# Performance work log

Hardware: AMD Instinct MI355X
Metric: run time of the kernel (lower is better)

The kernel has to match this reference:

```python
import jax, jax.numpy as jnp
import numpy as np
from jax import lax
import math

N_QUBITS = 10
N_LAYERS = 4
PI = jnp.float32(math.pi)


def _c(x):
    return x.astype(jnp.complex64)


def rx_mat(t):
    c = _c(jnp.cos(0.5 * t)); s = _c(jnp.sin(0.5 * t))
    return jnp.stack([jnp.stack([c, -1j * s]), jnp.stack([-1j * s, c])])


def ry_mat(t):
    c = _c(jnp.cos(0.5 * t)); s = _c(jnp.sin(0.5 * t))
    return jnp.stack([jnp.stack([c, -s]), jnp.stack([s, c])])


def rz_mat(t):
    e0 = jnp.exp(_c(jnp.zeros_like(t)) - 0.5j * _c(t))
    e1 = jnp.exp(0.5j * _c(t))
    z = jnp.zeros_like(e0)
    return jnp.stack([jnp.stack([e0, z]), jnp.stack([z, e1])])


def apply_1q(psi, U, q):
    # psi: (2,)*n complex, apply 2x2 U on axis q
    psi = jnp.moveaxis(psi, q, 0)
    psi = jnp.tensordot(U, psi, axes=(1, 0))
    return jnp.moveaxis(psi, 0, q)


def apply_cnot(psi, ctrl, tgt):
    psi = jnp.moveaxis(psi, (ctrl, tgt), (0, 1))
    a00, a01, a10, a11 = psi[0, 0], psi[0, 1], psi[1, 0], psi[1, 1]
    psi = jnp.stack([jnp.stack([a00, a01]), jnp.stack([a11, a10])])
    return jnp.moveaxis(psi, (0, 1), (ctrl, tgt))


def vqc(state, weights):
    # state: (D,) float32 angles; weights: (layers, n, 3)
    n, L = N_QUBITS, N_LAYERS
    D = state.shape[0]
    psi = jnp.full((2,) * n, 2.0 ** (-n / 2.0), dtype=jnp.complex64)  # H^n |0>
    for layer in range(L):
        for q in range(n):
            ang = state[(layer * n + q) % D]
            psi = apply_1q(psi, rx_mat(ang), q)
            psi = apply_1q(psi, ry_mat(ang), q)
            psi = apply_1q(psi, rz_mat(weights[layer, q, 0]), q)
            psi = apply_1q(psi, ry_mat(weights[layer, q, 1]), q)
            psi = apply_1q(psi, rz_mat(weights[layer, q, 2]), q)
        for q in range(n - 1):
            psi = apply_cnot(psi, q, q + 1)
        psi = apply_cnot(psi, n - 1, 0)
    probs = jnp.real(psi * jnp.conj(psi))  # (2,)*n
    zdiag = jnp.array([1.0, -1.0], dtype=jnp.float32)
    exps = [jnp.sum(probs * zdiag.reshape((1,) * q + (2,) + (1,) * (n - q - 1)))
            for q in range(n)]
    return jnp.stack(exps)  # (n,)


def lstm_forward(x, W_ih, W_hh, b_ih, b_hh):
    # x: [B,T,Din]; PyTorch gate order: i, f, g, o
    B, T, _ = x.shape
    H = W_hh.shape[1]
    b = b_ih + b_hh

    def step(carry, xt):
        h, c = carry
        gates = xt @ W_ih.T + h @ W_hh.T + b
        i, f, g, o = jnp.split(gates, 4, axis=-1)
        i = jax.nn.sigmoid(i); f = jax.nn.sigmoid(f)
        g = jnp.tanh(g); o = jax.nn.sigmoid(o)
        c = f * c + i * g
        h = o * jnp.tanh(c)
        return (h, c), h

    h0 = jnp.zeros((B, H), x.dtype)
    c0 = jnp.zeros((B, H), x.dtype)
    _, hs = lax.scan(step, (h0, c0), jnp.swapaxes(x, 0, 1))
    return jnp.swapaxes(hs, 0, 1)  # [B,T,H]


def _forward(s, lstm_s, W_ih, W_hh, b_ih, b_hh, proj_W, proj_b,
             in_proj_W, in_proj_b, out_proj_W, out_proj_b,
             qweights, W1, b1, W2, b2):
    hs = lstm_forward(lstm_s, W_ih, W_hh, b_ih, b_hh)      # [B,T,H]
    lstm_last = hs[:, -1, :]                               # [B,H]
    state_full = jnp.concatenate([lstm_last, s], axis=1)   # [B,E]
    lstm_proj = hs @ proj_W.T + proj_b                     # [B,T,E]
    E = proj_W.shape[0]
    Wq, Wk, Wv = in_proj_W[:E], in_proj_W[E:2 * E], in_proj_W[2 * E:]
    bq, bk, bv = in_proj_b[:E], in_proj_b[E:2 * E], in_proj_b[2 * E:]
    q = state_full @ Wq.T + bq                             # [B,E] (1 query token)
    k = lstm_proj @ Wk.T + bk                              # [B,T,E]
    v = lstm_proj @ Wv.T + bv
    scale = 1.0 / jnp.sqrt(jnp.float32(E))                 # num_heads=1 -> head_dim=E
    attn = jax.nn.softmax(jnp.einsum('be,bte->bt', q, k) * scale, axis=-1)
    ctx = jnp.einsum('bt,bte->be', attn, v)
    attn_out = ctx @ out_proj_W.T + out_proj_b             # [B,E]
    merged_state = jnp.concatenate([attn_out, s], axis=1)  # [B,E+F]
    state_norm = jnp.tanh(merged_state) * PI
    qfeat = jax.vmap(lambda st: vqc(st, qweights))(state_norm)  # [B,n]
    merged = jnp.concatenate([merged_state, qfeat], axis=1)
    x = jax.nn.relu(merged @ W1.T + b1)
    return x @ W2.T + b2


def setup_inputs() -> dict:
    key = jax.random.key(0)
    ks = jax.random.split(key, 16)
    B, T = 512, 256
    Din, H, F = 128, 256, 64
    E = H + F          # 320 = state_dim
    Dm = E + F         # 384 = merged_state dim
    n_l1, n_act = 512, 8

    def g(k, shape, std):
        return (std * jax.random.normal(k, shape)).astype(jnp.float32)

    return {
        's': jax.random.normal(ks[0], (B, F), jnp.float32),
        'lstm_s': jax.random.normal(ks[1], (B, T, Din), jnp.float32),
        'W_ih': g(ks[2], (4 * H, Din), 0.05),
        'W_hh': g(ks[3], (4 * H, H), 0.05),
        'b_ih': jnp.zeros((4 * H,), jnp.float32),
        'b_hh': jnp.zeros((4 * H,), jnp.float32),
        'proj_W': g(ks[4], (E, H), 0.05),
        'proj_b': 0.1 * jnp.ones((E,), jnp.float32),
        'in_proj_W': g(ks[5], (3 * E, E), 0.05),
        'in_proj_b': jnp.zeros((3 * E,), jnp.float32),
        'out_proj_W': g(ks[6], (E, E), 0.05),
        'out_proj_b': jnp.zeros((E,), jnp.float32),
        'qweights': jax.random.uniform(ks[7], (N_LAYERS, N_QUBITS, 3), jnp.float32, 0.0, 2.0 * math.pi),
        'W1': g(ks[8], (n_l1, Dm + N_QUBITS), 0.05),
        'b1': 0.1 * jnp.ones((n_l1,), jnp.float32),
        'W2': g(ks[9], (n_act, n_l1), 0.05),
        'b2': 0.1 * jnp.ones((n_act,), jnp.float32),
    }


def reference(s, lstm_s, W_ih, W_hh, b_ih, b_hh, proj_W, proj_b,
              in_proj_W, in_proj_b, out_proj_W, out_proj_b,
              qweights, W1, b1, W2, b2):
    return _forward(s, lstm_s, W_ih, W_hh, b_ih, b_hh, proj_W, proj_b,
                    in_proj_W, in_proj_b, out_proj_W, out_proj_b,
                    qweights, W1, b1, W2, b2)
```

## Files before the change

kernel.cpp:

```cpp
#include <hip/hip_runtime.h>
#include <hip/hip_bf16.h>
#include <math.h>

typedef unsigned int u32;
typedef unsigned long long u64;
typedef unsigned short u16;
typedef __attribute__((ext_vector_type(8))) short short8;
typedef __attribute__((ext_vector_type(4))) float f32x4;
typedef __attribute__((ext_vector_type(4))) int v4i;

#define PI_F 3.14159265358979f
#define B_   512
#define T_   256
#define DIN  128
#define H_   256
#define G4   1024
#define F_   64
#define E_   320
#define DM   384
#define NL1  512
#define NACT 8
#define KMLP 394

__device__ v4i llvm_amdgcn_raw_buffer_load_v4i32(v4i rsrc, int voffset,
                                                 int soffset, int aux)
    __asm("llvm.amdgcn.raw.buffer.load.v4i32");
__device__ void llvm_amdgcn_raw_buffer_store_i32(int vdata, v4i rsrc,
                                                 int voffset, int soffset,
                                                 int aux)
    __asm("llvm.amdgcn.raw.buffer.store.i32");

__device__ __forceinline__ v4i make_srd(const void* p) {
  v4i r;
  r.x = (int)(u32)(u64)p;
  r.y = (int)(u32)((u64)p >> 32);
  r.z = (int)0xFFFFFFFFu;
  r.w = 0x00020000;
  return r;
}

__device__ __forceinline__ float b2f(u16 h) {
  union { u32 u; float f; } v; v.u = ((u32)h) << 16; return v.f;
}
__device__ __forceinline__ u16 f2b(float f) {
  union { float f; u32 u; } v; v.f = f;
  u32 r = (v.u + 0x7FFFu + ((v.u >> 16) & 1u)) >> 16;
  return (u16)r;
}
__device__ __forceinline__ float sigf(float x) { return 1.0f / (1.0f + __expf(-x)); }
__device__ __forceinline__ float tanhfast(float x) { return 2.0f / (1.0f + __expf(-2.0f * x)) - 1.0f; }
__device__ __forceinline__ float2 cmul(float2 a, float2 b) {
  return make_float2(a.x * b.x - a.y * b.y, a.x * b.y + a.y * b.x);
}
__device__ __forceinline__ float2 cadd(float2 a, float2 b) {
  return make_float2(a.x + b.x, a.y + b.y);
}

__global__ void k_prep1(const float* __restrict__ lstm_s,
                        const float* __restrict__ W_ih,
                        const float* __restrict__ W_hh,
                        const float* __restrict__ b_ih,
                        const float* __restrict__ b_hh,
                        const float* __restrict__ ipw,
                        const float* __restrict__ ipb,
                        const float* __restrict__ projb,
                        const float* __restrict__ qw,
                        const float* __restrict__ W1,
                        u16* __restrict__ xbf,
                        u16* __restrict__ hs,
                        u16* __restrict__ Wg,
                        float* __restrict__ bb,
                        float* __restrict__ W1t,
                        float* __restrict__ uw,
                        float* __restrict__ bkp,
                        float* __restrict__ bvp,
                        u32* __restrict__ cnt) {
  const int bid = blockIdx.x;
  const int tid = threadIdx.x;
  if (bid < 8192) {
    u32 u = (u32)bid * 256u + tid;
    u32 c8 = u & 15u, b = (u >> 4) & 511u, t = u >> 13;
    const float* src = lstm_s + ((size_t)b * T_ + t) * DIN + c8 * 8;
    union { u16 h[8]; uint4 v; } tmp;
#pragma unroll
    for (int i = 0; i < 8; ++i) tmp.h[i] = f2b(src[i]);
    *(uint4*)(xbf + ((size_t)t * B_ + b) * DIN + c8 * 8) = tmp.v;
  } else if (bid < 8384) {
    u32 u = (u32)(bid - 8192) * 256u + tid;
    u32 c8 = u % 48u, r = u / 48u;
    const float* src = (c8 < 16) ? (W_ih + (size_t)r * DIN + c8 * 8)
                                 : (W_hh + (size_t)r * H_ + (c8 - 16) * 8);
    union { u16 h[8]; uint4 v; } tmp;
#pragma unroll
    for (int i = 0; i < 8; ++i) tmp.h[i] = f2b(src[i]);
    *(uint4*)(Wg + (size_t)r * 384 + c8 * 8) = tmp.v;
  } else if (bid < 8448) {
    u32 u = (u32)(bid - 8384) * 256u + tid;
    ((uint4*)hs)[u] = make_uint4(0, 0, 0, 0);
  } else if (bid < 9236) {
    u32 u = (u32)(bid - 8448) * 256u + tid;
    u32 k = u / 512u, nn = u % 512u;
    W1t[u] = W1[(size_t)nn * KMLP + k];
  } else if (bid == 9236) {
    for (int i = tid; i < 1024; i += 256) bb[i] = b_ih[i] + b_hh[i];
    for (int i = tid; i < 1024; i += 256) cnt[i] = 0u;
    if (tid < 40) {
      float w0 = qw[tid * 3 + 0], w1 = qw[tid * 3 + 1], w2 = qw[tid * 3 + 2];
      float c0 = cosf(0.5f * w0), s0 = sinf(0.5f * w0);
      float c1 = cosf(0.5f * w1), s1 = sinf(0.5f * w1);
      float c2 = cosf(0.5f * w2), s2 = sinf(0.5f * w2);
      float2 e0m = make_float2(c0, -s0), e0p = make_float2(c0, s0);
      float2 e2m = make_float2(c2, -s2), e2p = make_float2(c2, s2);
      float2 t00 = make_float2(c1 * e0m.x, c1 * e0m.y);
      float2 t01 = make_float2(-s1 * e0p.x, -s1 * e0p.y);
      float2 t10 = make_float2(s1 * e0m.x, s1 * e0m.y);
      float2 t11 = make_float2(c1 * e0p.x, c1 * e0p.y);
      float2 u00 = cmul(e2m, t00), u01 = cmul(e2m, t01);
      float2 u10 = cmul(e2p, t10), u11 = cmul(e2p, t11);
      float* o = uw + tid * 8;
      o[0] = u00.x; o[1] = u00.y; o[2] = u01.x; o[3] = u01.y;
      o[4] = u10.x; o[5] = u10.y; o[6] = u11.x; o[7] = u11.y;
    }
  } else if (bid <= 9238) {
    int o = (bid - 9237) * 256 + tid;
    if (o < E_) {
      float acc = ipb[E_ + o];
      for (int e = 0; e < E_; ++e) acc += ipw[(size_t)(E_ + o) * E_ + e] * projb[e];
      bkp[o] = acc;
    }
  } else {
    int o = (bid - 9239) * 256 + tid;
    if (o < E_) {
      float acc = ipb[2 * E_ + o];
      for (int e = 0; e < E_; ++e) acc += ipw[(size_t)(2 * E_ + o) * E_ + e] * projb[e];
      bvp[o] = acc;
    }
  }
}

__global__ void k_prep2(const float* __restrict__ ipw, const float* __restrict__ projW,
                        float* __restrict__ Wkp, float* __restrict__ Wvp) {
  int bid = blockIdx.x, tid = threadIdx.x;
  int o = (bid < 320) ? bid : (bid - 320);
  const float* wrow = ipw + (size_t)((bid < 320 ? E_ : 2 * E_) + o) * E_;
  float acc = 0.f;
  for (int e = 0; e < E_; ++e) acc += wrow[e] * projW[(size_t)e * H_ + tid];
  (bid < 320 ? Wkp : Wvp)[(size_t)o * H_ + tid] = acc;
}

__global__ void k_prep3(const float* __restrict__ ipw, const float* __restrict__ ipb,
                        const float* __restrict__ opw, const float* __restrict__ opb,
                        const float* __restrict__ Wkp, const float* __restrict__ Wvp,
                        const float* __restrict__ bkp, const float* __restrict__ bvp,
                        float* __restrict__ WuT, float* __restrict__ bu,
                        float* __restrict__ wd, float* __restrict__ ddp,
                        float* __restrict__ Wovt, float* __restrict__ bov) {
  int bid = blockIdx.x, tid = threadIdx.x;
  if (bid < 320) {
    int e = bid;
    float acc = 0.f;
    for (int o = 0; o < E_; ++o) acc += Wkp[(size_t)o * H_ + tid] * ipw[(size_t)o * E_ + e];
    WuT[(size_t)e * H_ + tid] = acc;
  } else if (bid < 576) {
    int jj = bid - 320;
    for (int i = tid; i < E_; i += 256) {
      float acc = 0.f;
      for (int o = 0; o < E_; ++o) acc += opw[(size_t)i * E_ + o] * Wvp[(size_t)o * H_ + jj];
      Wovt[(size_t)jj * E_ + i] = acc;
    }
  } else {
    {
      float acc = 0.f;
      for (int o = 0; o < E_; ++o) acc += Wkp[(size_t)o * H_ + tid] * ipb[o];
      bu[tid] = acc;
    }
    for (int idx = tid; idx < E_; idx += 256) {
      float a1 = 0.f, a2 = opb[idx];
      for (int o = 0; o < E_; ++o) {
        a1 += ipw[(size_t)o * E_ + idx] * bkp[o];
        a2 += opw[(size_t)idx * E_ + o] * bvp[o];
      }
      wd[idx] = a1; bov[idx] = a2;
    }
    if (tid == 0) {
      float acc = 0.f;
      for (int o = 0; o < E_; ++o) acc += ipb[o] * bkp[o];
      ddp[0] = acc;
    }
  }
}

struct LstmArgs {
  const u16* xbf; u16* hs; const u16* Wg; const float* bb; u32* cnt;
};

__launch_bounds__(256, 1)
__global__ void k_lstm(LstmArgs A) {
  const int g   = blockIdx.x & 7;
  const int n   = blockIdx.x >> 3;
  const int tid = threadIdx.x;
  const int wid = tid >> 6, lane = tid & 63;
  __shared__ __align__(16) u16 Wl[32 * 392];

  for (int idx = tid; idx < 32 * 48; idx += 256) {
    int ln = idx / 48, c8 = idx % 48;
    int gr = (ln >> 3) * 256 + n * 8 + (ln & 7);
    *(uint4*)&Wl[ln * 392 + c8 * 8] = *(const uint4*)&A.Wg[(size_t)gr * 384 + c8 * 8];
  }
  const int j  = lane & 7;
  const int gc = n * 8 + j;
  const float bbi = A.bb[gc], bbf2 = A.bb[256 + gc];
  const float bbg = A.bb[512 + gc], bbo = A.bb[768 + gc];

  const int quad = lane >> 4;
  const int mrow = lane & 15;
  const int brow = g * 64 + wid * 16 + mrow;
  const int erow0 = g * 64 + wid * 16 + quad * 4;
  const bool hi = (lane & 8) != 0;
  float crs[4] = {0.f, 0.f, 0.f, 0.f};
  u32* mycnt = A.cnt + g * 64;
  u32 target = 0;

  const v4i hs_srd = make_srd(A.hs);
  const int hvoff = (brow * H_ + quad * 8) * 2;

  uint4 xc0, xc1, xc2, xc3, xn0, xn1, xn2, xn3;
  {
    const u16* xb = A.xbf + ((size_t)0 * B_ + brow) * DIN + quad * 8;
    xc0 = *(const uint4*)(xb + 0);
    xc1 = *(const uint4*)(xb + 32);
    xc2 = *(const uint4*)(xb + 64);
    xc3 = *(const uint4*)(xb + 96);
  }
  __syncthreads();

  for (int t = 0; t < T_; ++t) {
    const int hsoff = t * (B_ * H_ * 2);
    uint4 h0 = __builtin_bit_cast(uint4, llvm_amdgcn_raw_buffer_load_v4i32(hs_srd, hvoff +   0, hsoff, 17));
    uint4 h1 = __builtin_bit_cast(uint4, llvm_amdgcn_raw_buffer_load_v4i32(hs_srd, hvoff +  64, hsoff, 17));
    uint4 h2 = __builtin_bit_cast(uint4, llvm_amdgcn_raw_buffer_load_v4i32(hs_srd, hvoff + 128, hsoff, 17));
    uint4 h3 = __builtin_bit_cast(uint4, llvm_amdgcn_raw_buffer_load_v4i32(hs_srd, hvoff + 192, hsoff, 17));
    uint4 h4 = __builtin_bit_cast(uint4, llvm_amdgcn_raw_buffer_load_v4i32(hs_srd, hvoff + 256, hsoff, 17));
    uint4 h5 = __builtin_bit_cast(uint4, llvm_amdgcn_raw_buffer_load_v4i32(hs_srd, hvoff + 320, hsoff, 17));
    uint4 h6 = __builtin_bit_cast(uint4, llvm_amdgcn_raw_buffer_load_v4i32(hs_srd, hvoff + 384, hsoff, 17));
    uint4 h7 = __builtin_bit_cast(uint4, llvm_amdgcn_raw_buffer_load_v4i32(hs_srd, hvoff + 448, hsoff, 17));
    {
      const int tn = (t + 1 < T_) ? (t + 1) : t;
      const u16* xb = A.xbf + ((size_t)tn * B_ + brow) * DIN + quad * 8;
      xn0 = *(const uint4*)(xb + 0);
      xn1 = *(const uint4*)(xb + 32);
      xn2 = *(const uint4*)(xb + 64);
      xn3 = *(const uint4*)(xb + 96);
    }

    f32x4 acc0 = {0.f, 0.f, 0.f, 0.f}, acc1 = {0.f, 0.f, 0.f, 0.f};
#define MMSTEP(AV, KOFF)                                                          \
    {                                                                             \
      short8 av  = __builtin_bit_cast(short8, AV);                                \
      short8 bv0 = __builtin_bit_cast(short8,                                     \
          *(const uint4*)&Wl[mrow * 392 + (KOFF) + quad * 8]);                    \
      short8 bv1 = __builtin_bit_cast(short8,                                     \
          *(const uint4*)&Wl[(16 + mrow) * 392 + (KOFF) + quad * 8]);             \
      acc0 = __builtin_amdgcn_mfma_f32_16x16x32_bf16(av, bv0, acc0, 0, 0, 0);     \
      acc1 = __builtin_amdgcn_mfma_f32_16x16x32_bf16(av, bv1, acc1, 0, 0, 0);     \
    }
    MMSTEP(xc0, 0)   MMSTEP(xc1, 32)  MMSTEP(xc2, 64)  MMSTEP(xc3, 96)
    MMSTEP(h0, 128)  MMSTEP(h1, 160)  MMSTEP(h2, 192)  MMSTEP(h3, 224)
    MMSTEP(h4, 256)  MMSTEP(h5, 288)  MMSTEP(h6, 320)  MMSTEP(h7, 352)
#undef MMSTEP

    const int hsoff_o = (t + 1) * (B_ * H_ * 2);
#pragma unroll
    for (int r = 0; r < 4; ++r) {
      float x0 = acc0[r], x1v = acc1[r];
      float y0 = __shfl_xor(x0, 8, 64);
      float y1 = __shfl_xor(x1v, 8, 64);
      float iv = (hi ? y0 : x0) + bbi;
      float fv = (hi ? x0 : y0) + bbf2;
      float gv = (hi ? y1 : x1v) + bbg;
      float ov = (hi ? x1v : y1) + bbo;
      float cc = sigf(fv) * crs[r] + sigf(iv) * tanhfast(gv);
      crs[r] = cc;
      float hh = sigf(ov) * tanhfast(cc);
      float hh2 = __shfl_xor(hh, 1, 64);
      if (!hi && ((j & 1) == 0)) {
        u32 pk = (u32)f2b(hh) | ((u32)f2b(hh2) << 16);
        llvm_amdgcn_raw_buffer_store_i32((int)pk, hs_srd,
                                         ((erow0 + r) * H_ + gc) * 2, hsoff_o, 17);
      }
    }
    target += 32;
    if (t != T_ - 1) {
      __syncthreads();
      if (tid == 0) {
        __hip_atomic_fetch_add(mycnt, 1u, __ATOMIC_RELAXED, __HIP_MEMORY_SCOPE_AGENT);
        int guard = 0;
        while (__hip_atomic_load(mycnt, __ATOMIC_RELAXED, __HIP_MEMORY_SCOPE_AGENT) < target) {
          __builtin_amdgcn_s_sleep(1);
          if (++guard > (1 << 24)) break;
        }
      }
      __syncthreads();
      xc0 = xn0; xc1 = xn1; xc2 = xn2; xc3 = xn3;
    }
  }
}

__global__ void k_u(const u16* __restrict__ hs, const float* __restrict__ s,
                    const float* __restrict__ WuT, const float* __restrict__ bu,
                    const float* __restrict__ wd, const float* __restrict__ ddp,
                    float* __restrict__ u, float* __restrict__ dvec) {
  int b = blockIdx.x, tid = threadIdx.x;
  __shared__ float z[E_];
  __shared__ float red[256];
  z[tid] = b2f(hs[((size_t)T_ * B_ + b) * H_ + tid]);
  if (tid < F_) z[H_ + tid] = s[(size_t)b * F_ + tid];
  __syncthreads();
  float acc = bu[tid];
  for (int e = 0; e < E_; ++e) acc += WuT[(size_t)e * H_ + tid] * z[e];
  u[(size_t)b * H_ + tid] = acc;
  float p = 0.f;
  for (int e = tid; e < E_; e += 256) p += wd[e] * z[e];
  red[tid] = p;
  __syncthreads();
  for (int s2 = 128; s2 > 0; s2 >>= 1) {
    if (tid < s2) red[tid] += red[tid + s2];
    __syncthreads();
  }
  if (tid == 0) dvec[b] = red[0] + ddp[0];
}

__global__ void k_aw(const u16* __restrict__ hs, const float* __restrict__ u,
                     const float* __restrict__ dvec, float* __restrict__ wv) {
  int b = blockIdx.x, tid = threadIdx.x;
  int wid = tid >> 6, lane = tid & 63;
  __shared__ float sc[T_];
  __shared__ float red[256];
  const float db = dvec[b];
  const float scale = 0.055901699437494745f;
  float4 ul = *(const float4*)&u[(size_t)b * H_ + lane * 4];
  for (int tt = 0; tt < 64; ++tt) {
    int t = wid * 64 + tt;
    u32 rw0 = ((const u32*)(hs + ((size_t)(t + 1) * B_ + b) * H_))[lane * 2];
    u32 rw1 = ((const u32*)(hs + ((size_t)(t + 1) * B_ + b) * H_))[lane * 2 + 1];
    union { u32 uu; float f; } f0, f1, f2, f3;
    f0.uu = rw0 << 16; f1.uu = rw0 & 0xFFFF0000u;
    f2.uu = rw1 << 16; f3.uu = rw1 & 0xFFFF0000u;
    float p = f0.f * ul.x + f1.f * ul.y + f2.f * ul.z + f3.f * ul.w;
#pragma unroll
    for (int off = 32; off > 0; off >>= 1) p += __shfl_xor(p, off, 64);
    if (lane == 0) sc[t] = (p + db) * scale;
  }
  __syncthreads();
  float v = sc[tid];
  red[tid] = v;
  __syncthreads();
  for (int s2 = 128; s2 > 0; s2 >>= 1) {
    if (tid < s2) red[tid] = fmaxf(red[tid], red[tid + s2]);
    __syncthreads();
  }
  float m = red[0];
  __syncthreads();
  float e = __expf(v - m);
  red[tid] = e;
  __syncthreads();
  for (int s2 = 128; s2 > 0; s2 >>= 1) {
    if (tid < s2) red[tid] += red[tid + s2];
    __syncthreads();
  }
  float inv = 1.f / red[0];
  __syncthreads();
  sc[tid] = e * inv;
  __syncthreads();
  float acc = 0.f;
#pragma unroll 8
  for (int t = 0; t < T_; ++t) {
    acc += sc[t] * b2f(hs[((size_t)(t + 1) * B_ + b) * H_ + tid]);
  }
  wv[(size_t)b * H_ + tid] = acc;
}

__global__ void k_ao(const float* __restrict__ wv, const float* __restrict__ Wovt,
                     const float* __restrict__ bov, const float* __restrict__ s,
                     float* __restrict__ mst) {
  int b = blockIdx.x, tid = threadIdx.x;
  __shared__ float wl[H_];
  if (tid < H_) wl[tid] = wv[(size_t)b * H_ + tid];
  __syncthreads();
  if (tid < E_) {
    float acc = bov[tid];
    for (int jj = 0; jj < H_; ++jj) acc += Wovt[(size_t)jj * E_ + tid] * wl[jj];
    mst[(size_t)b * DM + tid] = acc;
  } else if (tid < DM) {
    mst[(size_t)b * DM + tid] = s[(size_t)b * F_ + (tid - E_)];
  }
}

__global__ void k_vqc(const float* __restrict__ mst, const float* __restrict__ uwg,
                      float* __restrict__ qf) {
  int b = blockIdx.x, tid = threadIdx.x;
  __shared__ float2 psi[1024];
  __shared__ float ang[40];
  __shared__ float uwl[320];
  __shared__ float part[4][10];
  if (tid < 40) ang[tid] = tanhf(mst[(size_t)b * DM + tid]) * PI_F;
  uwl[tid] = uwg[tid];
  if (tid < 64) uwl[256 + tid] = uwg[256 + tid];
#pragma unroll
  for (int k = 0; k < 4; ++k) psi[tid + k * 256] = make_float2(0.03125f, 0.f);
  __syncthreads();
  for (int l = 0; l < 4; ++l) {
    for (int q = 0; q < 10; ++q) {
      int lq = l * 10 + q;
      float a = ang[lq];
      float ca = __cosf(0.5f * a), sa = __sinf(0.5f * a);
      float cs = ca * sa;
      float2 m00 = make_float2(ca * ca, sa * sa);
      float2 m01 = make_float2(-cs, -cs);
      float2 m10 = make_float2(cs, -cs);
      float2 m11 = make_float2(ca * ca, -sa * sa);
      const float* uwp = &uwl[lq * 8];
      float2 a00 = make_float2(uwp[0], uwp[1]), a01 = make_float2(uwp[2], uwp[3]);
      float2 a10 = make_float2(uwp[4], uwp[5]), a11 = make_float2(uwp[6], uwp[7]);
      float2 u00 = cadd(cmul(a00, m00), cmul(a01, m10));
      float2 u01 = cadd(cmul(a00, m01), cmul(a01, m11));
      float2 u10 = cadd(cmul(a10, m00), cmul(a11, m10));
      float2 u11 = cadd(cmul(a10, m01), cmul(a11, m11));
      int bp = 9 - q;
      __syncthreads();
#pragma unroll
      for (int k = 0; k < 2; ++k) {
        int p = tid + k * 256;
        int i0 = ((p >> bp) << (bp + 1)) | (p & ((1 << bp) - 1));
        int i1 = i0 | (1 << bp);
        float2 A0 = psi[i0], A1 = psi[i1];
        psi[i0] = cadd(cmul(u00, A0), cmul(u01, A1));
        psi[i1] = cadd(cmul(u10, A0), cmul(u11, A1));
      }
    }
    for (int q = 0; q < 9; ++q) {
      int lo = 8 - q;
      __syncthreads();
      int p = tid;
      int i0 = ((p >> lo) << (lo + 2)) | (2 << lo) | (p & ((1 << lo) - 1));
      int i1 = i0 | (1 << lo);
      float2 tmp = psi[i0]; psi[i0] = psi[i1]; psi[i1] = tmp;
    }
    __syncthreads();
    {
      int i0 = (tid << 1) | 1;
      int i1 = i0 | 512;
      float2 tmp = psi[i0]; psi[i0] = psi[i1]; psi[i1] = tmp;
    }
  }
  __syncthreads();
  float acc[10];
#pragma unroll
  for (int q = 0; q < 10; ++q) acc[q] = 0.f;
#pragma unroll
  for (int k = 0; k < 4; ++k) {
    int idx = tid + k * 256;
    float2 A = psi[idx];
    float pr = A.x * A.x + A.y * A.y;
#pragma unroll
    for (int q = 0; q < 10; ++q) acc[q] += ((idx >> (9 - q)) & 1) ? -pr : pr;
  }
  int lane = tid & 63, wid = tid >> 6;
#pragma unroll
  for (int q = 0; q < 10; ++q) {
    float vq = acc[q];
#pragma unroll
    for (int off = 32; off > 0; off >>= 1) vq += __shfl_xor(vq, off, 64);
    if (lane == 0) part[wid][q] = vq;
  }
  __syncthreads();
  if (tid < 10) qf[(size_t)b * 10 + tid] = part[0][tid] + part[1][tid] + part[2][tid] + part[3][tid];
}

__global__ void k_mlp(const float* __restrict__ mst, const float* __restrict__ qf,
                      const float* __restrict__ W1t, const float* __restrict__ b1,
                      const float* __restrict__ W2, const float* __restrict__ b2,
                      float* __restrict__ out) {
  int b = blockIdx.x, tid = threadIdx.x;
  __shared__ float mg[KMLP];
  __shared__ float x1[NL1];
  __shared__ float red[256];
  for (int i = tid; i < DM; i += 256) mg[i] = mst[(size_t)b * DM + i];
  if (tid < 10) mg[DM + tid] = qf[(size_t)b * 10 + tid];
  __syncthreads();
#pragma unroll
  for (int hh = 0; hh < 2; ++hh) {
    int nn = tid + hh * 256;
    float acc = b1[nn];
#pragma unroll 4
    for (int k = 0; k < KMLP; ++k) acc += W1t[(size_t)k * NL1 + nn] * mg[k];
    x1[nn] = fmaxf(acc, 0.f);
  }
  __syncthreads();
  int a = tid >> 5, l32 = tid & 31;
  float p = 0.f;
  for (int k = l32; k < NL1; k += 32) p += x1[k] * W2[(size_t)a * NL1 + k];
  red[tid] = p;
  __syncthreads();
  if (tid < 8) {
    float acc = b2[tid];
#pragma unroll
    for (int i = 0; i < 32; ++i) acc += red[tid * 32 + i];
    out[(size_t)b * NACT + tid] = acc;
  }
}

extern "C" void kernel_launch(void* const* d_in, const int* in_sizes, int n_in,
                              void* d_out, int out_size, void* d_ws, size_t ws_size,
                              hipStream_t stream) {
  const float* s      = (const float*)d_in[0];
  const float* lstm_s = (const float*)d_in[1];
  const float* W_ih   = (const float*)d_in[2];
  const float* W_hh   = (const float*)d_in[3];
  const float* b_ih   = (const float*)d_in[4];
  const float* b_hh   = (const float*)d_in[5];
  const float* projW  = (const float*)d_in[6];
  const float* projb  = (const float*)d_in[7];
  const float* ipw    = (const float*)d_in[8];
  const float* ipb    = (const float*)d_in[9];
  const float* opw    = (const float*)d_in[10];
  const float* opb    = (const float*)d_in[11];
  const float* qw     = (const float*)d_in[12];
  const float* W1     = (const float*)d_in[13];
  const float* b1     = (const float*)d_in[14];
  const float* W2     = (const float*)d_in[15];
  const float* b2     = (const float*)d_in[16];
  float* out = (float*)d_out;

  char* wsb = (char*)d_ws;
  size_t off = 0;
  auto alloc = [&](size_t bytes) -> void* {
    void* p = wsb + off;
    off = (off + bytes + 255) & ~(size_t)255;
    return p;
  };
  u16*  xbf  = (u16*)alloc((size_t)T_ * B_ * DIN * 2);
  u16*  hs   = (u16*)alloc((size_t)(T_ + 1) * B_ * H_ * 2);
  u16*  Wg   = (u16*)alloc((size_t)G4 * 384 * 2);
  float* bb  = (float*)alloc(G4 * 4);
  float* Wkp = (float*)alloc((size_t)E_ * H_ * 4);
  float* Wvp = (float*)alloc((size_t)E_ * H_ * 4);
  float* bkp = (float*)alloc(E_ * 4);
  float* bvp = (float*)alloc(E_ * 4);
  float* WuT = (float*)alloc((size_t)E_ * H_ * 4);
  float* bu  = (float*)alloc(H_ * 4);
  float* wd  = (float*)alloc(E_ * 4);
  float* ddp = (float*)alloc(256);
  float* Wovt= (float*)alloc((size_t)H_ * E_ * 4);
  float* bov = (float*)alloc(E_ * 4);
  float* uu  = (float*)alloc((size_t)B_ * H_ * 4);
  float* dvec= (float*)alloc(B_ * 4);
  float* wv  = (float*)alloc((size_t)B_ * H_ * 4);
  float* mst = (float*)alloc((size_t)B_ * DM * 4);
  float* qf  = (float*)alloc((size_t)B_ * 10 * 4);
  float* uw  = (float*)alloc(40 * 8 * 4);
  float* W1t = (float*)alloc((size_t)KMLP * NL1 * 4);
  u32*  cnt  = (u32*)alloc(1024 * 4);
  (void)ws_size; (void)in_sizes; (void)n_in; (void)out_size;

  hipLaunchKernelGGL(k_prep1, dim3(9241), dim3(256), 0, stream,
                     lstm_s, W_ih, W_hh, b_ih, b_hh, ipw, ipb, projb, qw, W1,
                     xbf, hs, Wg, bb, W1t, uw, bkp, bvp, cnt);
  hipLaunchKernelGGL(k_prep2, dim3(640), dim3(256), 0, stream, ipw, projW, Wkp, Wvp);
  hipLaunchKernelGGL(k_prep3, dim3(577), dim3(256), 0, stream,
                     ipw, ipb, opw, opb, Wkp, Wvp, bkp, bvp, WuT, bu, wd, ddp, Wovt, bov);

  LstmArgs la;
  la.xbf = xbf; la.hs = hs; la.Wg = Wg; la.bb = bb; la.cnt = cnt;
  void* kargs[] = { (void*)&la };
  hipError_t ce = hipLaunchCooperativeKernel(reinterpret_cast<const void*>(&k_lstm),
                                             dim3(256), dim3(256), kargs, 0, stream);
  if (ce != hipSuccess) {
    hipLaunchKernelGGL(k_lstm, dim3(256), dim3(256), 0, stream, la);
  }

  hipLaunchKernelGGL(k_u,   dim3(512), dim3(256), 0, stream, hs, s, WuT, bu, wd, ddp, uu, dvec);
  hipLaunchKernelGGL(k_aw,  dim3(512), dim3(256), 0, stream, hs, uu, dvec, wv);
  hipLaunchKernelGGL(k_ao,  dim3(512), dim3(384), 0, stream, wv, Wovt, bov, s, mst);
  hipLaunchKernelGGL(k_vqc, dim3(512), dim3(256), 0, stream, mst, uw, qf);
  hipLaunchKernelGGL(k_mlp, dim3(512), dim3(256), 0, stream, mst, qf, W1t, b1, W2, b2, out);
}
```

Baseline: 1.326 ms.

## Replace LSTM barrier with sentinel-polling on hidden state and fuse tail kernels

Removes the per-step counter barrier in the persistent LSTM kernel. The hidden-state buffer is now pre-filled with 0xFFFF bf16 sentinels, and each block spins reloading h until no word matches the sentinel, so consumers wait only on the data they actually read. To hide that wait, the x-projection MFMAs are issued before polling. The five tail kernels are merged into two (attention and VQC+MLP), which drops intermediate global buffers and launches. In exchange, k_prep1 must write sentinels over the whole hs buffer, the scheme relies on a real bf16 output never equalling 0xFFFF, and the glc polling loads add memory traffic.

```diff
diff --git a/kernel.cpp b/kernel.cpp
--- a/kernel.cpp
+++ b/kernel.cpp
@@ -54,6 +54,12 @@
 }
 __device__ __forceinline__ float2 cadd(float2 a, float2 b) {
   return make_float2(a.x + b.x, a.y + b.y);
+}
+__device__ __forceinline__ bool okw(u32 w) {
+  return ((w & 0xFFFFu) != 0xFFFFu) && ((w >> 16) != 0xFFFFu);
+}
+__device__ __forceinline__ bool ok4(uint4 v) {
+  return okw(v.x) & okw(v.y) & okw(v.z) & okw(v.w);
 }
 
 __global__ void k_prep1(const float* __restrict__ lstm_s,
@@ -94,14 +100,15 @@
 #pragma unroll
     for (int i = 0; i < 8; ++i) tmp.h[i] = f2b(src[i]);
     *(uint4*)(Wg + (size_t)r * 384 + c8 * 8) = tmp.v;
-  } else if (bid < 8448) {
+  } else if (bid < 24832) {
     u32 u = (u32)(bid - 8384) * 256u + tid;
-    ((uint4*)hs)[u] = make_uint4(0, 0, 0, 0);
-  } else if (bid < 9236) {
-    u32 u = (u32)(bid - 8448) * 256u + tid;
+    u32 v = (u < 16384u) ? 0u : 0xFFFFFFFFu;
+    ((uint4*)hs)[u] = make_uint4(v, v, v, v);
+  } else if (bid < 25620) {
+    u32 u = (u32)(bid - 24832) * 256u + tid;
     u32 k = u / 512u, nn = u % 512u;
     W1t[u] = W1[(size_t)nn * KMLP + k];
-  } else if (bid == 9236) {
+  } else if (bid == 25620) {
     for (int i = tid; i < 1024; i += 256) bb[i] = b_ih[i] + b_hh[i];
     for (int i = tid; i < 1024; i += 256) cnt[i] = 0u;
     if (tid < 40) {
@@ -121,15 +128,15 @@
       o[0] = u00.x; o[1] = u00.y; o[2] = u01.x; o[3] = u01.y;
       o[4] = u10.x; o[5] = u10.y; o[6] = u11.x; o[7] = u11.y;
     }
-  } else if (bid <= 9238) {
-    int o = (bid - 9237) * 256 + tid;
+  } else if (bid <= 25622) {
+    int o = (bid - 25621) * 256 + tid;
     if (o < E_) {
       float acc = ipb[E_ + o];
       for (int e = 0; e < E_; ++e) acc += ipw[(size_t)(E_ + o) * E_ + e] * projb[e];
       bkp[o] = acc;
     }
   } else {
-    int o = (bid - 9239) * 256 + tid;
+    int o = (bid - 25623) * 256 + tid;
     if (o < E_) {
       float acc = ipb[2 * E_ + o];
       for (int e = 0; e < E_; ++e) acc += ipw[(size_t)(2 * E_ + o) * E_ + e] * projb[e];
@@ -218,8 +225,6 @@
   const int erow0 = g * 64 + wid * 16 + quad * 4;
   const bool hi = (lane & 8) != 0;
   float crs[4] = {0.f, 0.f, 0.f, 0.f};
-  u32* mycnt = A.cnt + g * 64;
-  u32 target = 0;
 
   const v4i hs_srd = make_srd(A.hs);
   const int hvoff = (brow * H_ + quad * 8) * 2;
@@ -234,26 +239,6 @@
   }
   __syncthreads();
 
-  for (int t = 0; t < T_; ++t) {
-    const int hsoff = t * (B_ * H_ * 2);
-    uint4 h0 = __builtin_bit_cast(uint4, llvm_amdgcn_raw_buffer_load_v4i32(hs_srd, hvoff +   0, hsoff, 17));
-    uint4 h1 = __builtin_bit_cast(uint4, llvm_amdgcn_raw_buffer_load_v4i32(hs_srd, hvoff +  64, hsoff, 17));
-    uint4 h2 = __builtin_bit_cast(uint4, llvm_amdgcn_raw_buffer_load_v4i32(hs_srd, hvoff + 128, hsoff, 17));
-    uint4 h3 = __builtin_bit_cast(uint4, llvm_amdgcn_raw_buffer_load_v4i32(hs_srd, hvoff + 192, hsoff, 17));
-    uint4 h4 = __builtin_bit_cast(uint4, llvm_amdgcn_raw_buffer_load_v4i32(hs_srd, hvoff + 256, hsoff, 17));
-    uint4 h5 = __builtin_bit_cast(uint4, llvm_amdgcn_raw_buffer_load_v4i32(hs_srd, hvoff + 320, hsoff, 17));
-    uint4 h6 = __builtin_bit_cast(uint4, llvm_amdgcn_raw_buffer_load_v4i32(hs_srd, hvoff + 384, hsoff, 17));
-    uint4 h7 = __builtin_bit_cast(uint4, llvm_amdgcn_raw_buffer_load_v4i32(hs_srd, hvoff + 448, hsoff, 17));
-    {
-      const int tn = (t + 1 < T_) ? (t + 1) : t;
-      const u16* xb = A.xbf + ((size_t)tn * B_ + brow) * DIN + quad * 8;
-      xn0 = *(const uint4*)(xb + 0);
-      xn1 = *(const uint4*)(xb + 32);
-      xn2 = *(const uint4*)(xb + 64);
-      xn3 = *(const uint4*)(xb + 96);
-    }
-
-    f32x4 acc0 = {0.f, 0.f, 0.f, 0.f}, acc1 = {0.f, 0.f, 0.f, 0.f};
 #define MMSTEP(AV, KOFF)                                                          \
     {                                                                             \
       short8 av  = __builtin_bit_cast(short8, AV);                                \
@@ -264,10 +249,41 @@
       acc0 = __builtin_amdgcn_mfma_f32_16x16x32_bf16(av, bv0, acc0, 0, 0, 0);     \
       acc1 = __builtin_amdgcn_mfma_f32_16x16x32_bf16(av, bv1, acc1, 0, 0, 0);     \
     }
+
+  for (int t = 0; t < T_; ++t) {
+    {
+      const int tn = (t + 1 < T_) ? (t + 1) : t;
+      const u16* xb = A.xbf + ((size_t)tn * B_ + brow) * DIN + quad * 8;
+      xn0 = *(const uint4*)(xb + 0);
+      xn1 = *(const uint4*)(xb + 32);
+      xn2 = *(const uint4*)(xb + 64);
+      xn3 = *(const uint4*)(xb + 96);
+    }
+
+    f32x4 acc0 = {0.f, 0.f, 0.f, 0.f}, acc1 = {0.f, 0.f, 0.f, 0.f};
     MMSTEP(xc0, 0)   MMSTEP(xc1, 32)  MMSTEP(xc2, 64)  MMSTEP(xc3, 96)
+
+    const int hsoff = t * (B_ * H_ * 2);
+    uint4 h0, h1, h2, h3, h4, h5, h6, h7;
+    int it = 0;
+    for (;;) {
+      asm volatile("" ::: "memory");
+      h0 = __builtin_bit_cast(uint4, llvm_amdgcn_raw_buffer_load_v4i32(hs_srd, hvoff +   0, hsoff, 17));
+      h1 = __builtin_bit_cast(uint4, llvm_amdgcn_raw_buffer_load_v4i32(hs_srd, hvoff +  64, hsoff, 17));
+      h2 = __builtin_bit_cast(uint4, llvm_amdgcn_raw_buffer_load_v4i32(hs_srd, hvoff + 128, hsoff, 17));
+      h3 = __builtin_bit_cast(uint4, llvm_amdgcn_raw_buffer_load_v4i32(hs_srd, hvoff + 192, hsoff, 17));
+      h4 = __builtin_bit_cast(uint4, llvm_amdgcn_raw_buffer_load_v4i32(hs_srd, hvoff + 256, hsoff, 17));
+      h5 = __builtin_bit_cast(uint4, llvm_amdgcn_raw_buffer_load_v4i32(hs_srd, hvoff + 320, hsoff, 17));
+      h6 = __builtin_bit_cast(uint4, llvm_amdgcn_raw_buffer_load_v4i32(hs_srd, hvoff + 384, hsoff, 17));
+      h7 = __builtin_bit_cast(uint4, llvm_amdgcn_raw_buffer_load_v4i32(hs_srd, hvoff + 448, hsoff, 17));
+      bool v = ok4(h0) & ok4(h1) & ok4(h2) & ok4(h3) &
+               ok4(h4) & ok4(h5) & ok4(h6) & ok4(h7);
+      if (__all(v)) break;
+      if (++it > (1 << 16)) break;
+    }
+
     MMSTEP(h0, 128)  MMSTEP(h1, 160)  MMSTEP(h2, 192)  MMSTEP(h3, 224)
     MMSTEP(h4, 256)  MMSTEP(h5, 288)  MMSTEP(h6, 320)  MMSTEP(h7, 352)
-#undef MMSTEP
 
     const int hsoff_o = (t + 1) * (B_ * H_ * 2);
 #pragma unroll
@@ -289,56 +305,48 @@
                                          ((erow0 + r) * H_ + gc) * 2, hsoff_o, 17);
       }
     }
-    target += 32;
-    if (t != T_ - 1) {
-      __syncthreads();
-      if (tid == 0) {
-        __hip_atomic_fetch_add(mycnt, 1u, __ATOMIC_RELAXED, __HIP_MEMORY_SCOPE_AGENT);
-        int guard = 0;
-        while (__hip_atomic_load(mycnt, __ATOMIC_RELAXED, __HIP_MEMORY_SCOPE_AGENT) < target) {
-          __builtin_amdgcn_s_sleep(1);
-          if (++guard > (1 << 24)) break;
-        }
-      }
-      __syncthreads();
-      xc0 = xn0; xc1 = xn1; xc2 = xn2; xc3 = xn3;
-    }
-  }
-}
-
-__global__ void k_u(const u16* __restrict__ hs, const float* __restrict__ s,
-                    const float* __restrict__ WuT, const float* __restrict__ bu,
-                    const float* __restrict__ wd, const float* __restrict__ ddp,
-                    float* __restrict__ u, float* __restrict__ dvec) {
+    xc0 = xn0; xc1 = xn1; xc2 = xn2; xc3 = xn3;
+  }
+#undef MMSTEP
+}
+
+__global__ void k_attn(const u16* __restrict__ hs, const float* __restrict__ s,
+                       const float* __restrict__ WuT, const float* __restrict__ bu,
+                       const float* __restrict__ wd, const float* __restrict__ ddp,
+                       const float* __restrict__ Wovt, const float* __restrict__ bov,
+                       float* __restrict__ mst) {
   int b = blockIdx.x, tid = threadIdx.x;
+  int wid = tid >> 6, lane = tid & 63;
   __shared__ float z[E_];
   __shared__ float red[256];
+  __shared__ float sc[T_];
+  __shared__ float uvec[H_];
+  __shared__ float wl[H_];
+  __shared__ float dsh;
   z[tid] = b2f(hs[((size_t)T_ * B_ + b) * H_ + tid]);
   if (tid < F_) z[H_ + tid] = s[(size_t)b * F_ + tid];
   __syncthreads();
-  float acc = bu[tid];
-  for (int e = 0; e < E_; ++e) acc += WuT[(size_t)e * H_ + tid] * z[e];
-  u[(size_t)b * H_ + tid] = acc;
-  float p = 0.f;
-  for (int e = tid; e < E_; e += 256) p += wd[e] * z[e];
-  red[tid] = p;
+  {
+    float acc = bu[tid];
+    for (int e = 0; e < E_; ++e) acc += WuT[(size_t)e * H_ + tid] * z[e];
+    uvec[tid] = acc;
+  }
+  {
+    float p = 0.f;
+    for (int e = tid; e < E_; e += 256) p += wd[e] * z[e];
+    red[tid] = p;
+  }
   __syncthreads();
   for (int s2 = 128; s2 > 0; s2 >>= 1) {
     if (tid < s2) red[tid] += red[tid + s2];
     __syncthreads();
   }
-  if (tid == 0) dvec[b] = red[0] + ddp[0];
-}
-
-__global__ void k_aw(const u16* __restrict__ hs, const float* __restrict__ u,
-                     const float* __restrict__ dvec, float* __restrict__ wv) {
-  int b = blockIdx.x, tid = threadIdx.x;
-  int wid = tid >> 6, lane = tid & 63;
-  __shared__ float sc[T_];
-  __shared__ float red[256];
-  const float db = dvec[b];
+  if (tid == 0) dsh = red[0] + ddp[0];
+  __syncthreads();
+  const float db = dsh;
   const float scale = 0.055901699437494745f;
-  float4 ul = *(const float4*)&u[(size_t)b * H_ + lane * 4];
+  float4 ul = make_float4(uvec[lane * 4], uvec[lane * 4 + 1],
+                          uvec[lane * 4 + 2], uvec[lane * 4 + 3]);
   for (int tt = 0; tt < 64; ++tt) {
     int t = wid * 64 + tt;
     u32 rw0 = ((const u32*)(hs + ((size_t)(t + 1) * B_ + b) * H_))[lane * 2];
@@ -372,37 +380,36 @@
   __syncthreads();
   sc[tid] = e * inv;
   __syncthreads();
-  float acc = 0.f;
+  {
+    float acc = 0.f;
 #pragma unroll 8
-  for (int t = 0; t < T_; ++t) {
-    acc += sc[t] * b2f(hs[((size_t)(t + 1) * B_ + b) * H_ + tid]);
-  }
-  wv[(size_t)b * H_ + tid] = acc;
-}
-
-__global__ void k_ao(const float* __restrict__ wv, const float* __restrict__ Wovt,
-                     const float* __restrict__ bov, const float* __restrict__ s,
-                     float* __restrict__ mst) {
-  int b = blockIdx.x, tid = threadIdx.x;
-  __shared__ float wl[H_];
-  if (tid < H_) wl[tid] = wv[(size_t)b * H_ + tid];
-  __syncthreads();
-  if (tid < E_) {
-    float acc = bov[tid];
-    for (int jj = 0; jj < H_; ++jj) acc += Wovt[(size_t)jj * E_ + tid] * wl[jj];
-    mst[(size_t)b * DM + tid] = acc;
-  } else if (tid < DM) {
-    mst[(size_t)b * DM + tid] = s[(size_t)b * F_ + (tid - E_)];
-  }
-}
-
-__global__ void k_vqc(const float* __restrict__ mst, const float* __restrict__ uwg,
-                      float* __restrict__ qf) {
+    for (int t = 0; t < T_; ++t) {
+      acc += sc[t] * b2f(hs[((size_t)(t + 1) * B_ + b) * H_ + tid]);
+    }
+    wl[tid] = acc;
+  }
+  __syncthreads();
+  for (int i = tid; i < E_; i += 256) {
+    float a2 = bov[i];
+    for (int jj = 0; jj < H_; ++jj) a2 += Wovt[(size_t)jj * E_ + i] * wl[jj];
+    mst[(size_t)b * DM + i] = a2;
+  }
+  if (tid < F_) mst[(size_t)b * DM + E_ + tid] = s[(size_t)b * F_ + tid];
+}
+
+__global__ void k_vqcmlp(const float* __restrict__ mst, const float* __restrict__ uwg,
+                         const float* __restrict__ W1t, const float* __restrict__ b1,
+                         const float* __restrict__ W2, const float* __restrict__ b2,
+                         float* __restrict__ out) {
   int b = blockIdx.x, tid = threadIdx.x;
   __shared__ float2 psi[1024];
   __shared__ float ang[40];
   __shared__ float uwl[320];
   __shared__ float part[4][10];
+  __shared__ float qfl[10];
+  __shared__ float mg[KMLP];
+  __shared__ float x1[NL1];
+  __shared__ float red[256];
   if (tid < 40) ang[tid] = tanhf(mst[(size_t)b * DM + tid]) * PI_F;
   uwl[tid] = uwg[tid];
   if (tid < 64) uwl[256 + tid] = uwg[256 + tid];
@@ -474,27 +481,18 @@
     if (lane == 0) part[wid][q] = vq;
   }
   __syncthreads();
-  if (tid < 10) qf[(size_t)b * 10 + tid] = part[0][tid] + part[1][tid] + part[2][tid] + part[3][tid];
-}
-
-__global__ void k_mlp(const float* __restrict__ mst, const float* __restrict__ qf,
-                      const float* __restrict__ W1t, const float* __restrict__ b1,
-                      const float* __restrict__ W2, const float* __restrict__ b2,
-                      float* __restrict__ out) {
-  int b = blockIdx.x, tid = threadIdx.x;
-  __shared__ float mg[KMLP];
-  __shared__ float x1[NL1];
-  __shared__ float red[256];
+  if (tid < 10) qfl[tid] = part[0][tid] + part[1][tid] + part[2][tid] + part[3][tid];
   for (int i = tid; i < DM; i += 256) mg[i] = mst[(size_t)b * DM + i];
-  if (tid < 10) mg[DM + tid] = qf[(size_t)b * 10 + tid];
+  __syncthreads();
+  if (tid < 10) mg[DM + tid] = qfl[tid];
   __syncthreads();
 #pragma unroll
   for (int hh = 0; hh < 2; ++hh) {
     int nn = tid + hh * 256;
-    float acc = b1[nn];
+    float a1 = b1[nn];
 #pragma unroll 4
-    for (int k = 0; k < KMLP; ++k) acc += W1t[(size_t)k * NL1 + nn] * mg[k];
-    x1[nn] = fmaxf(acc, 0.f);
+    for (int k = 0; k < KMLP; ++k) a1 += W1t[(size_t)k * NL1 + nn] * mg[k];
+    x1[nn] = fmaxf(a1, 0.f);
   }
   __syncthreads();
   int a = tid >> 5, l32 = tid & 31;
@@ -503,10 +501,10 @@
   red[tid] = p;
   __syncthreads();
   if (tid < 8) {
-    float acc = b2[tid];
-#pragma unroll
-    for (int i = 0; i < 32; ++i) acc += red[tid * 32 + i];
-    out[(size_t)b * NACT + tid] = acc;
+    float a2 = b2[tid];
+#pragma unroll
+    for (int i = 0; i < 32; ++i) a2 += red[tid * 32 + i];
+    out[(size_t)b * NACT + tid] = a2;
   }
 }
 
@@ -553,17 +551,13 @@
   float* ddp = (float*)alloc(256);
   float* Wovt= (float*)alloc((size_t)H_ * E_ * 4);
   float* bov = (float*)alloc(E_ * 4);
-  float* uu  = (float*)alloc((size_t)B_ * H_ * 4);
-  float* dvec= (float*)alloc(B_ * 4);
-  float* wv  = (float*)alloc((size_t)B_ * H_ * 4);
   float* mst = (float*)alloc((size_t)B_ * DM * 4);
-  float* qf  = (float*)alloc((size_t)B_ * 10 * 4);
   float* uw  = (float*)alloc(40 * 8 * 4);
   float* W1t = (float*)alloc((size_t)KMLP * NL1 * 4);
   u32*  cnt  = (u32*)alloc(1024 * 4);
   (void)ws_size; (void)in_sizes; (void)n_in; (void)out_size;
 
-  hipLaunchKernelGGL(k_prep1, dim3(9241), dim3(256), 0, stream,
+  hipLaunchKernelGGL(k_prep1, dim3(25625), dim3(256), 0, stream,
                      lstm_s, W_ih, W_hh, b_ih, b_hh, ipw, ipb, projb, qw, W1,
                      xbf, hs, Wg, bb, W1t, uw, bkp, bvp, cnt);
   hipLaunchKernelGGL(k_prep2, dim3(640), dim3(256), 0, stream, ipw, projW, Wkp, Wvp);
@@ -579,9 +573,8 @@
     hipLaunchKernelGGL(k_lstm, dim3(256), dim3(256), 0, stream, la);
   }
 
-  hipLaunchKernelGGL(k_u,   dim3(512), dim3(256), 0, stream, hs, s, WuT, bu, wd, ddp, uu, dvec);
-  hipLaunchKernelGGL(k_aw,  dim3(512), dim3(256), 0, stream, hs, uu, dvec, wv);
-  hipLaunchKernelGGL(k_ao,  dim3(512), dim3(384), 0, stream, wv, Wovt, bov, s, mst);
-  hipLaunchKernelGGL(k_vqc, dim3(512), dim3(256), 0, stream, mst, uw, qf);
-  hipLaunchKernelGGL(k_mlp, dim3(512), dim3(256), 0, stream, mst, qf, W1t, b1, W2, b2, out);
-}
+  hipLaunchKernelGGL(k_attn,   dim3(512), dim3(256), 0, stream,
+                     hs, s, WuT, bu, wd, ddp, Wovt, bov, mst);
+  hipLaunchKernelGGL(k_vqcmlp, dim3(512), dim3(256), 0, stream,
+                     mst, uw, W1t, b1, W2, b2, out);
+}
```

Measured after the change: 1.925 ms. 45.1% more time.
